# Performance work log

Measured on AMD Instinct MI355X. Metric: run time of the kernel, lower is better.

The kernel has to match this reference:

```python
import jax, jax.numpy as jnp
import numpy as np
from functools import partial

THRESHOLD = 2.0  # CannyEdgeNet(threshold=2.0)

# ---- fixed (non-learned) Canny filters, as in CannyEdgePytorch ----

def _gaussian_1d(size=5, std=1.0):
    x = np.arange(size) - (size - 1) / 2.0
    g = np.exp(-0.5 * (x / std) ** 2)
    g = g / g.sum()
    return g.astype(np.float32)

_G = _gaussian_1d(5, 1.0)
GAUSS_H = jnp.asarray(_G.reshape(1, 1, 1, 5))   # (O,I,kh,kw)
GAUSS_V = jnp.asarray(_G.reshape(1, 1, 5, 1))
_SOBEL = np.array([[1, 0, -1], [2, 0, -2], [1, 0, -1]], dtype=np.float32)
SOBEL_H = jnp.asarray(_SOBEL.reshape(1, 1, 3, 3))      # d/dx
SOBEL_V = jnp.asarray(_SOBEL.T.reshape(1, 1, 3, 3))    # d/dy
# 8 orientation-NMS filters: center minus neighbor at 0,45,...,315 degrees
_DIRS = np.zeros((8, 1, 3, 3), dtype=np.float32)
_NBR = [(1, 2), (2, 2), (2, 1), (2, 0), (1, 0), (0, 0), (0, 1), (0, 2)]
for _k, (_r, _c) in enumerate(_NBR):
    _DIRS[_k, 0, 1, 1] = 1.0
    _DIRS[_k, 0, _r, _c] = -1.0
DIR_FILTERS = jnp.asarray(_DIRS)

_DN = ('NCHW', 'OIHW', 'NCHW')

def _conv(x, w, pad):
    return jax.lax.conv_general_dilated(x, w, (1, 1), pad, dimension_numbers=_DN)


def canny_thresholded(img):
    """img: [N,3,H,W] -> thresholded thin edges [N,1,H,W]."""
    N, C, H, W = img.shape
    x = img.reshape(N * C, 1, H, W)
    # separable gaussian blur (per channel)
    blur = _conv(_conv(x, GAUSS_H, [(0, 0), (2, 2)]), GAUSS_V, [(2, 2), (0, 0)])
    gx = _conv(blur, SOBEL_H, [(1, 1), (1, 1)]).reshape(N, C, H, W)
    gy = _conv(blur, SOBEL_V, [(1, 1), (1, 1)]).reshape(N, C, H, W)
    # per-channel magnitudes summed over RGB, as in the original
    grad_mag = jnp.sqrt(gx * gx + gy * gy).sum(axis=1, keepdims=True)  # [N,1,H,W]
    gx_s = gx.sum(axis=1, keepdims=True)
    gy_s = gy.sum(axis=1, keepdims=True)
    ori = jnp.arctan2(gy_s, gx_s) * (180.0 / np.pi) + 180.0
    ori = jnp.round(ori / 45.0) * 45.0
    # orientation-dependent non-maximum suppression
    all_filtered = _conv(grad_mag, DIR_FILTERS, [(1, 1), (1, 1)])  # [N,8,H,W]
    idx_pos = jnp.mod(ori / 45.0, 8.0).astype(jnp.int32)            # [N,1,H,W]
    idx_neg = jnp.mod(ori / 45.0 + 4.0, 8.0).astype(jnp.int32)
    pos = jnp.take_along_axis(all_filtered, idx_pos, axis=1)
    neg = jnp.take_along_axis(all_filtered, idx_neg, axis=1)
    is_max = jnp.minimum(pos, neg) > 0.0
    thin = jnp.where(is_max, grad_mag, 0.0)
    thresholded = jnp.where(thin < THRESHOLD, 0.0, thin)
    return thresholded


def setup_inputs() -> dict:
    key = jax.random.key(0)
    k1, k2 = jax.random.split(key)
    shape = (4, 16, 3, 256, 256)  # [B, T, C, H, W]
    data_input = jax.random.uniform(k1, shape, dtype=jnp.float32)
    model_output = jax.random.uniform(k2, shape, dtype=jnp.float32)
    return {"data_input": data_input, "model_output": model_output}


def reference(data_input, model_output):
    B, T, C, H, W = data_input.shape
    tgt = data_input.reshape(B * T, C, H, W)
    out = model_output.reshape(B * T, C, H, W)
    # edge extraction is under torch.no_grad() in the original
    e_out = jax.lax.stop_gradient(canny_thresholded(out))
    e_tgt = jax.lax.stop_gradient(canny_thresholded(tgt))
    # mean over per-frame L1 losses == global mean (all frames equal size)
    return jnp.mean(jnp.abs(e_out - e_tgt))
```

## Files before the change

kernel.cpp:

```cpp
#include <hip/hip_runtime.h>
#include <math.h>

#define HW   256
#define TR   16
#define TC   32
#define NBLK 8192
#define BR   24
#define HC   36
#define VR   20
#define GR   18
#define GC   34
#define GCP  35
#define NHALO 100
#define NG1  (BR * 9)
#define NG2  (VR * 9)

typedef float f32x2 __attribute__((ext_vector_type(2)));

namespace {
constexpr double kE2  = 0.13533528323661269189;
constexpr double kE05 = 0.60653065971263342360;
constexpr double kSum = 1.0 + 2.0 * kE2 + 2.0 * kE05;
constexpr float G0f = (float)(kE2 / kSum);
constexpr float G1f = (float)(kE05 / kSum);
constexpr float G2f = (float)(1.0 / kSum);
constexpr float T1  = 0.41421356237309503f;
constexpr float T2  = 2.41421356237309503f;
__device__ __forceinline__ float fast_sqrtf(float x) {
    return __builtin_amdgcn_sqrtf(x);
}
__device__ __forceinline__ int iclamp(int v, int lo, int hi) {
    return v < lo ? lo : (v > hi ? hi : v);
}
__device__ __forceinline__ f32x2 mk2(float x, float y) {
    f32x2 r; r.x = x; r.y = y; return r;
}
}

template<bool EDGE>
__device__ __forceinline__ float tile_body(
    const float* __restrict__ bA, const float* __restrict__ bB,
    const int tid, const int ty0, const int tx0,
    float* __restrict__ s_tmp, float* __restrict__ s_blur,
    float* __restrict__ s_grad)
{
    const int ox  = tid & 31;
    const int oy0 = (tid >> 5) * 2;

    const f32x2 g0p = mk2(G0f, G0f), g1p = mk2(G1f, G1f), g2p = mk2(G2f, G2f);

    const int  q9  = tid / 9;
    const int  c4  = (tid - 9 * q9) * 4;
    const int  stw = q9 * HC + c4;
    const bool a1on = (tid < NG1);
    const int  y1   = ty0 - 4 + q9;
    const bool y1ok = !EDGE || ((unsigned)y1 < HW);
    const int  x0   = tx0 - 4 + c4;
    const int  ga   = y1 * HW + (EDGE ? iclamp(x0, 0, HW - 4) : x0);
    const int  gb   = y1 * HW + (EDGE ? iclamp(x0 + 4, 0, HW - 4) : x0 + 4);
    const bool a2on = (tid < NG2);
    const int  y2   = ty0 - 2 + q9;
    const bool y2ok = !EDGE || ((unsigned)y2 < HW);
    const int  xb2  = tx0 - 2 + c4;
    const bool ok0 = !EDGE || ((unsigned)(xb2 + 0) < HW);
    const bool ok1 = !EDGE || ((unsigned)(xb2 + 1) < HW);
    const bool ok2 = !EDGE || ((unsigned)(xb2 + 2) < HW);
    const bool ok3 = !EDGE || ((unsigned)(xb2 + 3) < HW);
    const int  b3  = (oy0 + 1) * HC + (ox + 1);
    const int  gw  = (oy0 + 1) * GCP + (ox + 1);
    int h_r = 0, h_cc = 0;
    if (tid < 34)        { h_r = 0;            h_cc = tid; }
    else if (tid < 68)   { h_r = GR - 1;       h_cc = tid - 34; }
    else if (tid < 84)   { h_r = tid - 68 + 1; h_cc = 0; }
    else if (tid < NHALO){ h_r = tid - 84 + 1; h_cc = GC - 1; }
    const bool has_halo = (tid < NHALO);
    const bool h_in = !EDGE || (((unsigned)(ty0 - 1 + h_r) < HW) &&
                                ((unsigned)(tx0 - 1 + h_cc) < HW));
    const int  h_b  = h_r * HC + h_cc;
    const int  h_gw = h_r * GCP + h_cc;

    f32x2 e_first = mk2(0.f, 0.f);
    float acc = 0.0f;

    for (int img = 0; img < 2; ++img) {
        const float* base = (img == 0) ? bA : bB;
        f32x2 gxs2 = mk2(0.f, 0.f), gys2 = mk2(0.f, 0.f), gms2 = mk2(0.f, 0.f);
        float hmag = 0.0f;

        for (int c = 0; c < 3; ++c) {
            const float* plane = base + c * (HW * HW);

            if (a1on) {
                float4 o = make_float4(0.f, 0.f, 0.f, 0.f);
                if (y1ok) {
                    const float4 a = *(const float4*)(plane + ga);
                    const float4 b = *(const float4*)(plane + gb);
                    const f32x2 p0 = mk2(a.x, a.y), p1 = mk2(a.y, a.z);
                    const f32x2 p2 = mk2(a.z, a.w), p3 = mk2(a.w, b.x);
                    const f32x2 p4 = mk2(b.x, b.y);
                    const f32x2 q3 = mk2(b.y, b.z), q4 = mk2(b.z, b.w);
                    const f32x2 oxy = g0p*p0 + g1p*p1 + g2p*p2 + g1p*p3 + g0p*p4;
                    const f32x2 ozw = g0p*p2 + g1p*p3 + g2p*p4 + g1p*q3 + g0p*q4;
                    o.x = oxy.x; o.y = oxy.y; o.z = ozw.x; o.w = ozw.y;
                    if (EDGE) {
                        if (x0 < 0) {
                            o.x = G0f*a.x;
                            o.y = G1f*a.x + G0f*a.y;
                            o.z = G2f*a.x + G1f*a.y + G0f*a.z;
                            o.w = G1f*a.x + G2f*a.y + G1f*a.z + G0f*a.w;
                        } else if (x0 > HW - 8) {
                            o.x = G0f*a.x + G1f*a.y + G2f*a.z + G1f*a.w;
                            o.y = G0f*a.y + G1f*a.z + G2f*a.w;
                            o.z = G0f*a.z + G1f*a.w;
                            o.w = G0f*a.w;
                        }
                    }
                }
                *(float4*)&s_tmp[stw] = o;
            }
            __syncthreads();

            if (a2on) {
                float4 v = make_float4(0.f, 0.f, 0.f, 0.f);
                if (y2ok) {
                    const float4 t0 = *(const float4*)&s_tmp[stw];
                    const float4 t1 = *(const float4*)&s_tmp[stw + 1 * HC];
                    const float4 t2 = *(const float4*)&s_tmp[stw + 2 * HC];
                    const float4 t3 = *(const float4*)&s_tmp[stw + 3 * HC];
                    const float4 t4 = *(const float4*)&s_tmp[stw + 4 * HC];
                    const f32x2 vxy = g0p*mk2(t0.x,t0.y) + g1p*mk2(t1.x,t1.y)
                                    + g2p*mk2(t2.x,t2.y) + g1p*mk2(t3.x,t3.y)
                                    + g0p*mk2(t4.x,t4.y);
                    const f32x2 vzw = g0p*mk2(t0.z,t0.w) + g1p*mk2(t1.z,t1.w)
                                    + g2p*mk2(t2.z,t2.w) + g1p*mk2(t3.z,t3.w)
                                    + g0p*mk2(t4.z,t4.w);
                    v.x = ok0 ? vxy.x : 0.f;
                    v.y = ok1 ? vxy.y : 0.f;
                    v.z = ok2 ? vzw.x : 0.f;
                    v.w = ok3 ? vzw.y : 0.f;
                }
                *(float4*)&s_blur[stw] = v;
            }
            __syncthreads();

            {
                float cd[4], rs[4];
                #pragma unroll
                for (int r = 0; r < 4; ++r) {
                    const float* b = &s_blur[b3 + r * HC];
                    const float bl = b[0], bc = b[1], br = b[2];
                    cd[r] = bl - br;
                    rs[r] = bl + 2.0f * bc + br;
                }
                const f32x2 gx2 = mk2(cd[0], cd[1]) + 2.0f * mk2(cd[1], cd[2])
                                + mk2(cd[2], cd[3]);
                const f32x2 gy2 = mk2(rs[0], rs[1]) - mk2(rs[2], rs[3]);
                gxs2 += gx2;
                gys2 += gy2;
                const f32x2 m2 = gx2 * gx2 + gy2 * gy2;
                gms2 += mk2(fast_sqrtf(m2.x), fast_sqrtf(m2.y));
                s_grad[gw]       = gms2.x;
                s_grad[gw + GCP] = gms2.y;
            }

            if (has_halo) {
                float gmag = 0.0f;
                if (h_in) {
                    const float* b = &s_blur[h_b];
                    const float b00 = b[0],        b01 = b[1],          b02 = b[2];
                    const float b10 = b[HC],                            b12 = b[HC + 2];
                    const float b20 = b[2 * HC],   b21 = b[2 * HC + 1], b22 = b[2 * HC + 2];
                    const float gx = (b00 + 2.0f * b10 + b20) - (b02 + 2.0f * b12 + b22);
                    const float gy = (b00 + 2.0f * b01 + b02) - (b20 + 2.0f * b21 + b22);
                    gmag = fast_sqrtf(gx * gx + gy * gy);
                }
                hmag += gmag;
                s_grad[h_gw] = hmag;
            }
        }
        __syncthreads();

        f32x2 e2;
        #pragma unroll
        for (int k = 0; k < 2; ++k) {
            const float gc = (k == 0) ? gms2.x : gms2.y;
            const float gx = (k == 0) ? gxs2.x : gxs2.y;
            const float gy = (k == 0) ? gys2.x : gys2.y;
            const float ax = fabsf(gx), ay = fabsf(gy);
            int dy, dx;
            if (ay <= T1 * ax)      { dy = 0; dx = 1; }
            else if (ay >= T2 * ax) { dy = 1; dx = 0; }
            else                    { dy = 1; dx = ((gx > 0.0f) == (gy > 0.0f)) ? 1 : -1; }
            const int ci = gw + k * GCP;
            const float pos = gc - s_grad[ci + dy * GCP + dx];
            const float neg = gc - s_grad[ci - dy * GCP - dx];
            const float thin = (fminf(pos, neg) > 0.0f) ? gc : 0.0f;
            const float e    = (thin < 2.0f) ? 0.0f : thin;
            if (k == 0) e2.x = e; else e2.y = e;
        }
        if (img == 0) e_first = e2;
        else          acc += fabsf(e2.x - e_first.x) + fabsf(e2.y - e_first.y);
        __syncthreads();
    }
    return acc;
}

__global__ __launch_bounds__(256, 8)
void canny_tile_kernel(const float* __restrict__ imgA,
                       const float* __restrict__ imgB,
                       float* __restrict__ partials)
{
    __shared__ __align__(16) float s_tmp[BR * HC];
    __shared__ __align__(16) float s_blur[VR * HC];
    __shared__ float s_grad[GR * GCP];
    __shared__ float s_red[4];

    const int tid = threadIdx.x;
    const int bid = blockIdx.x;
    const int lg  = (bid & 7) * (NBLK / 8) + (bid >> 3);
    const int n    = lg >> 7;
    const int tile = lg & 127;
    const int rt   = tile >> 3;
    const int ct   = tile & 7;
    const int ty0  = rt * TR;
    const int tx0  = ct * TC;

    const float* bA = imgA + (size_t)n * 3 * (HW * HW);
    const float* bB = imgB + (size_t)n * 3 * (HW * HW);

    const bool interior = (rt >= 1) && (rt <= 14) && (ct >= 1) && (ct <= 6);

    float acc;
    if (interior) acc = tile_body<false>(bA, bB, tid, ty0, tx0, s_tmp, s_blur, s_grad);
    else          acc = tile_body<true >(bA, bB, tid, ty0, tx0, s_tmp, s_blur, s_grad);

    #pragma unroll
    for (int off = 32; off > 0; off >>= 1) acc += __shfl_down(acc, off, 64);
    if ((tid & 63) == 0) s_red[tid >> 6] = acc;
    __syncthreads();
    if (tid == 0) partials[bid] = (s_red[0] + s_red[1]) + (s_red[2] + s_red[3]);
}

__global__ void final_reduce_kernel(const float* __restrict__ partials,
                                    float* __restrict__ out)
{
    __shared__ float s_red[16];
    const int tid = threadIdx.x;
    const float4 a = *(const float4*)&partials[4 * tid];
    const float4 b = *(const float4*)&partials[4 * tid + 4096];
    float v = ((a.x + a.y) + (a.z + a.w)) + ((b.x + b.y) + (b.z + b.w));
    #pragma unroll
    for (int off = 32; off > 0; off >>= 1) v += __shfl_down(v, off, 64);
    if ((tid & 63) == 0) s_red[tid >> 6] = v;
    __syncthreads();
    if (tid == 0) {
        float s = 0.0f;
        #pragma unroll
        for (int j = 0; j < 16; ++j) s += s_red[j];
        out[0] = s * (1.0f / 4194304.0f);
    }
}

extern "C" void kernel_launch(void* const* d_in, const int* in_sizes, int n_in,
                              void* d_out, int out_size, void* d_ws, size_t ws_size,
                              hipStream_t stream)
{
    const float* tgt     = (const float*)d_in[0];
    const float* out_img = (const float*)d_in[1];
    float* partials = (float*)d_ws;

    canny_tile_kernel<<<NBLK, 256, 0, stream>>>(out_img, tgt, partials);
    final_reduce_kernel<<<1, 1024, 0, stream>>>(partials, (float*)d_out);
}
```

Measured before the change: 47.06 us.

## Double tile height to 32 rows with four outputs per thread

Tile height grows from 16 to 32 rows, halving the block count. Each thread now makes two passes through the horizontal and vertical blur stages and computes four output rows instead of two. This cuts the relative halo overhead: fewer redundant global loads and blur work for overlapping rows. It also drops the trailing barrier at the end of each image iteration. In exchange there is more register pressure, a larger shared-memory footprint, and fewer blocks to spread across CUs.

```diff
diff --git a/kernel.cpp b/kernel.cpp
--- a/kernel.cpp
+++ b/kernel.cpp
@@ -2,16 +2,16 @@
 #include <math.h>
 
 #define HW   256
-#define TR   16
+#define TR   32
 #define TC   32
-#define NBLK 8192
-#define BR   24
+#define NBLK 4096
+#define BR   40
 #define HC   36
-#define VR   20
-#define GR   18
+#define VR   36
+#define GR   34
 #define GC   34
 #define GCP  35
-#define NHALO 100
+#define NHALO 132
 #define NG1  (BR * 9)
 #define NG2  (VR * 9)
 
@@ -45,122 +45,142 @@
     float* __restrict__ s_grad)
 {
     const int ox  = tid & 31;
-    const int oy0 = (tid >> 5) * 2;
+    const int oy0 = (tid >> 5) * 4;
 
     const f32x2 g0p = mk2(G0f, G0f), g1p = mk2(G1f, G1f), g2p = mk2(G2f, G2f);
 
-    const int  q9  = tid / 9;
-    const int  c4  = (tid - 9 * q9) * 4;
-    const int  stw = q9 * HC + c4;
-    const bool a1on = (tid < NG1);
-    const int  y1   = ty0 - 4 + q9;
-    const bool y1ok = !EDGE || ((unsigned)y1 < HW);
-    const int  x0   = tx0 - 4 + c4;
-    const int  ga   = y1 * HW + (EDGE ? iclamp(x0, 0, HW - 4) : x0);
-    const int  gb   = y1 * HW + (EDGE ? iclamp(x0 + 4, 0, HW - 4) : x0 + 4);
-    const bool a2on = (tid < NG2);
-    const int  y2   = ty0 - 2 + q9;
-    const bool y2ok = !EDGE || ((unsigned)y2 < HW);
-    const int  xb2  = tx0 - 2 + c4;
-    const bool ok0 = !EDGE || ((unsigned)(xb2 + 0) < HW);
-    const bool ok1 = !EDGE || ((unsigned)(xb2 + 1) < HW);
-    const bool ok2 = !EDGE || ((unsigned)(xb2 + 2) < HW);
-    const bool ok3 = !EDGE || ((unsigned)(xb2 + 3) < HW);
+    int  stw[2], ga[2], gb[2], x0v[2];
+    bool y1ok[2], y2ok[2], okc[2][4];
+    #pragma unroll
+    for (int j = 0; j < 2; ++j) {
+        const int gg = tid + j * 256;
+        const int r  = gg / 9;
+        const int c4 = (gg - 9 * r) * 4;
+        stw[j] = r * HC + c4;
+        const int y1 = ty0 - 4 + r;
+        y1ok[j] = !EDGE || ((unsigned)y1 < HW);
+        const int x0 = tx0 - 4 + c4;
+        x0v[j] = x0;
+        ga[j] = y1 * HW + (EDGE ? iclamp(x0, 0, HW - 4) : x0);
+        gb[j] = y1 * HW + (EDGE ? iclamp(x0 + 4, 0, HW - 4) : x0 + 4);
+        const int y2 = ty0 - 2 + r;
+        y2ok[j] = !EDGE || ((unsigned)y2 < HW);
+        const int xb2 = tx0 - 2 + c4;
+        #pragma unroll
+        for (int t = 0; t < 4; ++t)
+            okc[j][t] = !EDGE || ((unsigned)(xb2 + t) < HW);
+    }
     const int  b3  = (oy0 + 1) * HC + (ox + 1);
     const int  gw  = (oy0 + 1) * GCP + (ox + 1);
     int h_r = 0, h_cc = 0;
-    if (tid < 34)        { h_r = 0;            h_cc = tid; }
-    else if (tid < 68)   { h_r = GR - 1;       h_cc = tid - 34; }
-    else if (tid < 84)   { h_r = tid - 68 + 1; h_cc = 0; }
-    else if (tid < NHALO){ h_r = tid - 84 + 1; h_cc = GC - 1; }
+    if (tid < 34)        { h_r = 0;             h_cc = tid; }
+    else if (tid < 68)   { h_r = GR - 1;        h_cc = tid - 34; }
+    else if (tid < 100)  { h_r = tid - 68 + 1;  h_cc = 0; }
+    else if (tid < NHALO){ h_r = tid - 100 + 1; h_cc = GC - 1; }
     const bool has_halo = (tid < NHALO);
     const bool h_in = !EDGE || (((unsigned)(ty0 - 1 + h_r) < HW) &&
                                 ((unsigned)(tx0 - 1 + h_cc) < HW));
     const int  h_b  = h_r * HC + h_cc;
     const int  h_gw = h_r * GCP + h_cc;
 
-    f32x2 e_first = mk2(0.f, 0.f);
+    float e_first[4];
     float acc = 0.0f;
 
     for (int img = 0; img < 2; ++img) {
         const float* base = (img == 0) ? bA : bB;
-        f32x2 gxs2 = mk2(0.f, 0.f), gys2 = mk2(0.f, 0.f), gms2 = mk2(0.f, 0.f);
+        f32x2 gxs01 = mk2(0.f,0.f), gxs23 = mk2(0.f,0.f);
+        f32x2 gys01 = mk2(0.f,0.f), gys23 = mk2(0.f,0.f);
+        f32x2 gms01 = mk2(0.f,0.f), gms23 = mk2(0.f,0.f);
         float hmag = 0.0f;
 
         for (int c = 0; c < 3; ++c) {
             const float* plane = base + c * (HW * HW);
 
-            if (a1on) {
-                float4 o = make_float4(0.f, 0.f, 0.f, 0.f);
-                if (y1ok) {
-                    const float4 a = *(const float4*)(plane + ga);
-                    const float4 b = *(const float4*)(plane + gb);
-                    const f32x2 p0 = mk2(a.x, a.y), p1 = mk2(a.y, a.z);
-                    const f32x2 p2 = mk2(a.z, a.w), p3 = mk2(a.w, b.x);
-                    const f32x2 p4 = mk2(b.x, b.y);
-                    const f32x2 q3 = mk2(b.y, b.z), q4 = mk2(b.z, b.w);
-                    const f32x2 oxy = g0p*p0 + g1p*p1 + g2p*p2 + g1p*p3 + g0p*p4;
-                    const f32x2 ozw = g0p*p2 + g1p*p3 + g2p*p4 + g1p*q3 + g0p*q4;
-                    o.x = oxy.x; o.y = oxy.y; o.z = ozw.x; o.w = ozw.y;
-                    if (EDGE) {
-                        if (x0 < 0) {
-                            o.x = G0f*a.x;
-                            o.y = G1f*a.x + G0f*a.y;
-                            o.z = G2f*a.x + G1f*a.y + G0f*a.z;
-                            o.w = G1f*a.x + G2f*a.y + G1f*a.z + G0f*a.w;
-                        } else if (x0 > HW - 8) {
-                            o.x = G0f*a.x + G1f*a.y + G2f*a.z + G1f*a.w;
-                            o.y = G0f*a.y + G1f*a.z + G2f*a.w;
-                            o.z = G0f*a.z + G1f*a.w;
-                            o.w = G0f*a.w;
+            #pragma unroll
+            for (int j = 0; j < 2; ++j) {
+                if (j == 0 || tid < NG1 - 256) {
+                    float4 o = make_float4(0.f, 0.f, 0.f, 0.f);
+                    if (y1ok[j]) {
+                        const float4 a = *(const float4*)(plane + ga[j]);
+                        const float4 b = *(const float4*)(plane + gb[j]);
+                        const f32x2 p0 = mk2(a.x, a.y), p1 = mk2(a.y, a.z);
+                        const f32x2 p2 = mk2(a.z, a.w), p3 = mk2(a.w, b.x);
+                        const f32x2 p4 = mk2(b.x, b.y);
+                        const f32x2 q3 = mk2(b.y, b.z), q4 = mk2(b.z, b.w);
+                        const f32x2 oxy = g0p*p0 + g1p*p1 + g2p*p2 + g1p*p3 + g0p*p4;
+                        const f32x2 ozw = g0p*p2 + g1p*p3 + g2p*p4 + g1p*q3 + g0p*q4;
+                        o.x = oxy.x; o.y = oxy.y; o.z = ozw.x; o.w = ozw.y;
+                        if (EDGE) {
+                            if (x0v[j] < 0) {
+                                o.x = G0f*a.x;
+                                o.y = G1f*a.x + G0f*a.y;
+                                o.z = G2f*a.x + G1f*a.y + G0f*a.z;
+                                o.w = G1f*a.x + G2f*a.y + G1f*a.z + G0f*a.w;
+                            } else if (x0v[j] > HW - 8) {
+                                o.x = G0f*a.x + G1f*a.y + G2f*a.z + G1f*a.w;
+                                o.y = G0f*a.y + G1f*a.z + G2f*a.w;
+                                o.z = G0f*a.z + G1f*a.w;
+                                o.w = G0f*a.w;
+                            }
                         }
                     }
-                }
-                *(float4*)&s_tmp[stw] = o;
+                    *(float4*)&s_tmp[stw[j]] = o;
+                }
             }
             __syncthreads();
 
-            if (a2on) {
-                float4 v = make_float4(0.f, 0.f, 0.f, 0.f);
-                if (y2ok) {
-                    const float4 t0 = *(const float4*)&s_tmp[stw];
-                    const float4 t1 = *(const float4*)&s_tmp[stw + 1 * HC];
-                    const float4 t2 = *(const float4*)&s_tmp[stw + 2 * HC];
-                    const float4 t3 = *(const float4*)&s_tmp[stw + 3 * HC];
-                    const float4 t4 = *(const float4*)&s_tmp[stw + 4 * HC];
-                    const f32x2 vxy = g0p*mk2(t0.x,t0.y) + g1p*mk2(t1.x,t1.y)
-                                    + g2p*mk2(t2.x,t2.y) + g1p*mk2(t3.x,t3.y)
-                                    + g0p*mk2(t4.x,t4.y);
-                    const f32x2 vzw = g0p*mk2(t0.z,t0.w) + g1p*mk2(t1.z,t1.w)
-                                    + g2p*mk2(t2.z,t2.w) + g1p*mk2(t3.z,t3.w)
-                                    + g0p*mk2(t4.z,t4.w);
-                    v.x = ok0 ? vxy.x : 0.f;
-                    v.y = ok1 ? vxy.y : 0.f;
-                    v.z = ok2 ? vzw.x : 0.f;
-                    v.w = ok3 ? vzw.y : 0.f;
-                }
-                *(float4*)&s_blur[stw] = v;
+            #pragma unroll
+            for (int j = 0; j < 2; ++j) {
+                if (j == 0 || tid < NG2 - 256) {
+                    float4 v = make_float4(0.f, 0.f, 0.f, 0.f);
+                    if (y2ok[j]) {
+                        const int w = stw[j];
+                        const float4 t0 = *(const float4*)&s_tmp[w];
+                        const float4 t1 = *(const float4*)&s_tmp[w + 1 * HC];
+                        const float4 t2 = *(const float4*)&s_tmp[w + 2 * HC];
+                        const float4 t3 = *(const float4*)&s_tmp[w + 3 * HC];
+                        const float4 t4 = *(const float4*)&s_tmp[w + 4 * HC];
+                        const f32x2 vxy = g0p*mk2(t0.x,t0.y) + g1p*mk2(t1.x,t1.y)
+                                        + g2p*mk2(t2.x,t2.y) + g1p*mk2(t3.x,t3.y)
+                                        + g0p*mk2(t4.x,t4.y);
+                        const f32x2 vzw = g0p*mk2(t0.z,t0.w) + g1p*mk2(t1.z,t1.w)
+                                        + g2p*mk2(t2.z,t2.w) + g1p*mk2(t3.z,t3.w)
+                                        + g0p*mk2(t4.z,t4.w);
+                        v.x = okc[j][0] ? vxy.x : 0.f;
+                        v.y = okc[j][1] ? vxy.y : 0.f;
+                        v.z = okc[j][2] ? vzw.x : 0.f;
+                        v.w = okc[j][3] ? vzw.y : 0.f;
+                    }
+                    *(float4*)&s_blur[stw[j]] = v;
+                }
             }
             __syncthreads();
 
             {
-                float cd[4], rs[4];
+                float cd[6], rs[6];
                 #pragma unroll
-                for (int r = 0; r < 4; ++r) {
+                for (int r = 0; r < 6; ++r) {
                     const float* b = &s_blur[b3 + r * HC];
                     const float bl = b[0], bc = b[1], br = b[2];
                     cd[r] = bl - br;
                     rs[r] = bl + 2.0f * bc + br;
                 }
-                const f32x2 gx2 = mk2(cd[0], cd[1]) + 2.0f * mk2(cd[1], cd[2])
-                                + mk2(cd[2], cd[3]);
-                const f32x2 gy2 = mk2(rs[0], rs[1]) - mk2(rs[2], rs[3]);
-                gxs2 += gx2;
-                gys2 += gy2;
-                const f32x2 m2 = gx2 * gx2 + gy2 * gy2;
-                gms2 += mk2(fast_sqrtf(m2.x), fast_sqrtf(m2.y));
-                s_grad[gw]       = gms2.x;
-                s_grad[gw + GCP] = gms2.y;
+                const f32x2 gx01 = mk2(cd[0], cd[1]) + 2.0f * mk2(cd[1], cd[2])
+                                 + mk2(cd[2], cd[3]);
+                const f32x2 gx23 = mk2(cd[2], cd[3]) + 2.0f * mk2(cd[3], cd[4])
+                                 + mk2(cd[4], cd[5]);
+                const f32x2 gy01 = mk2(rs[0], rs[1]) - mk2(rs[2], rs[3]);
+                const f32x2 gy23 = mk2(rs[2], rs[3]) - mk2(rs[4], rs[5]);
+                gxs01 += gx01; gxs23 += gx23;
+                gys01 += gy01; gys23 += gy23;
+                const f32x2 m01 = gx01 * gx01 + gy01 * gy01;
+                const f32x2 m23 = gx23 * gx23 + gy23 * gy23;
+                gms01 += mk2(fast_sqrtf(m01.x), fast_sqrtf(m01.y));
+                gms23 += mk2(fast_sqrtf(m23.x), fast_sqrtf(m23.y));
+                s_grad[gw]           = gms01.x;
+                s_grad[gw + GCP]     = gms01.y;
+                s_grad[gw + 2 * GCP] = gms23.x;
+                s_grad[gw + 3 * GCP] = gms23.y;
             }
 
             if (has_halo) {
@@ -180,12 +200,13 @@
         }
         __syncthreads();
 
-        f32x2 e2;
+        const float gcv[4] = {gms01.x, gms01.y, gms23.x, gms23.y};
+        const float gxv[4] = {gxs01.x, gxs01.y, gxs23.x, gxs23.y};
+        const float gyv[4] = {gys01.x, gys01.y, gys23.x, gys23.y};
         #pragma unroll
-        for (int k = 0; k < 2; ++k) {
-            const float gc = (k == 0) ? gms2.x : gms2.y;
-            const float gx = (k == 0) ? gxs2.x : gxs2.y;
-            const float gy = (k == 0) ? gys2.x : gys2.y;
+        for (int k = 0; k < 4; ++k) {
+            const float gc = gcv[k];
+            const float gx = gxv[k], gy = gyv[k];
             const float ax = fabsf(gx), ay = fabsf(gy);
             int dy, dx;
             if (ay <= T1 * ax)      { dy = 0; dx = 1; }
@@ -196,11 +217,9 @@
             const float neg = gc - s_grad[ci - dy * GCP - dx];
             const float thin = (fminf(pos, neg) > 0.0f) ? gc : 0.0f;
             const float e    = (thin < 2.0f) ? 0.0f : thin;
-            if (k == 0) e2.x = e; else e2.y = e;
+            if (img == 0) e_first[k] = e;
+            else          acc += fabsf(e - e_first[k]);
         }
-        if (img == 0) e_first = e2;
-        else          acc += fabsf(e2.x - e_first.x) + fabsf(e2.y - e_first.y);
-        __syncthreads();
     }
     return acc;
 }
@@ -218,8 +237,8 @@
     const int tid = threadIdx.x;
     const int bid = blockIdx.x;
     const int lg  = (bid & 7) * (NBLK / 8) + (bid >> 3);
-    const int n    = lg >> 7;
-    const int tile = lg & 127;
+    const int n    = lg >> 6;
+    const int tile = lg & 63;
     const int rt   = tile >> 3;
     const int ct   = tile & 7;
     const int ty0  = rt * TR;
@@ -228,7 +247,7 @@
     const float* bA = imgA + (size_t)n * 3 * (HW * HW);
     const float* bB = imgB + (size_t)n * 3 * (HW * HW);
 
-    const bool interior = (rt >= 1) && (rt <= 14) && (ct >= 1) && (ct <= 6);
+    const bool interior = (rt >= 1) && (rt <= 6) && (ct >= 1) && (ct <= 6);
 
     float acc;
     if (interior) acc = tile_body<false>(bA, bB, tid, ty0, tx0, s_tmp, s_blur, s_grad);
@@ -247,8 +266,7 @@
     __shared__ float s_red[16];
     const int tid = threadIdx.x;
     const float4 a = *(const float4*)&partials[4 * tid];
-    const float4 b = *(const float4*)&partials[4 * tid + 4096];
-    float v = ((a.x + a.y) + (a.z + a.w)) + ((b.x + b.y) + (b.z + b.w));
+    float v = (a.x + a.y) + (a.z + a.w);
     #pragma unroll
     for (int off = 32; off > 0; off >>= 1) v += __shfl_down(v, off, 64);
     if ((tid & 63) == 0) s_red[tid >> 6] = v;
```

Measured after the change: 50.95 us. +8.3%, slower.

## Process both images concurrently per channel with duplicated shared buffers

Applied to the files above, without the earlier changes.

Replaces the sequential two-image loop with a single channel loop that handles image A and image B side by side, using separate shared-memory buffers for each. This halves the number of block-wide barriers and issues twice as many independent global loads and ALU operations between barriers, which exposes more instruction-level parallelism. In exchange, LDS use per block roughly doubles and register pressure rises, which may lower occupancy under the 8-blocks-per-SM launch bound.

```diff
diff --git a/kernel.cpp b/kernel.cpp
--- a/kernel.cpp
+++ b/kernel.cpp
@@ -41,8 +41,9 @@
 __device__ __forceinline__ float tile_body(
     const float* __restrict__ bA, const float* __restrict__ bB,
     const int tid, const int ty0, const int tx0,
-    float* __restrict__ s_tmp, float* __restrict__ s_blur,
-    float* __restrict__ s_grad)
+    float* __restrict__ s_tmpA,  float* __restrict__ s_tmpB,
+    float* __restrict__ s_blurA, float* __restrict__ s_blurB,
+    float* __restrict__ s_gradA, float* __restrict__ s_gradB)
 {
     const int ox  = tid & 31;
     const int oy0 = (tid >> 5) * 2;
@@ -79,128 +80,209 @@
     const int  h_b  = h_r * HC + h_cc;
     const int  h_gw = h_r * GCP + h_cc;
 
-    f32x2 e_first = mk2(0.f, 0.f);
-    float acc = 0.0f;
-
-    for (int img = 0; img < 2; ++img) {
-        const float* base = (img == 0) ? bA : bB;
-        f32x2 gxs2 = mk2(0.f, 0.f), gys2 = mk2(0.f, 0.f), gms2 = mk2(0.f, 0.f);
-        float hmag = 0.0f;
-
-        for (int c = 0; c < 3; ++c) {
-            const float* plane = base + c * (HW * HW);
-
-            if (a1on) {
-                float4 o = make_float4(0.f, 0.f, 0.f, 0.f);
-                if (y1ok) {
-                    const float4 a = *(const float4*)(plane + ga);
-                    const float4 b = *(const float4*)(plane + gb);
-                    const f32x2 p0 = mk2(a.x, a.y), p1 = mk2(a.y, a.z);
-                    const f32x2 p2 = mk2(a.z, a.w), p3 = mk2(a.w, b.x);
-                    const f32x2 p4 = mk2(b.x, b.y);
-                    const f32x2 q3 = mk2(b.y, b.z), q4 = mk2(b.z, b.w);
+    f32x2 gxsA = mk2(0.f,0.f), gysA = mk2(0.f,0.f), gmsA = mk2(0.f,0.f);
+    f32x2 gxsB = mk2(0.f,0.f), gysB = mk2(0.f,0.f), gmsB = mk2(0.f,0.f);
+    float hmA = 0.f, hmB = 0.f;
+
+    for (int c = 0; c < 3; ++c) {
+        const float* pA = bA + c * (HW * HW);
+        const float* pB = bB + c * (HW * HW);
+
+        if (a1on) {
+            float4 oA = make_float4(0.f,0.f,0.f,0.f);
+            float4 oB = make_float4(0.f,0.f,0.f,0.f);
+            if (y1ok) {
+                const float4 aA = *(const float4*)(pA + ga);
+                const float4 bA4 = *(const float4*)(pA + gb);
+                const float4 aB = *(const float4*)(pB + ga);
+                const float4 bB4 = *(const float4*)(pB + gb);
+                {
+                    const f32x2 p0 = mk2(aA.x, aA.y), p1 = mk2(aA.y, aA.z);
+                    const f32x2 p2 = mk2(aA.z, aA.w), p3 = mk2(aA.w, bA4.x);
+                    const f32x2 p4 = mk2(bA4.x, bA4.y);
+                    const f32x2 q3 = mk2(bA4.y, bA4.z), q4 = mk2(bA4.z, bA4.w);
                     const f32x2 oxy = g0p*p0 + g1p*p1 + g2p*p2 + g1p*p3 + g0p*p4;
                     const f32x2 ozw = g0p*p2 + g1p*p3 + g2p*p4 + g1p*q3 + g0p*q4;
-                    o.x = oxy.x; o.y = oxy.y; o.z = ozw.x; o.w = ozw.y;
-                    if (EDGE) {
-                        if (x0 < 0) {
-                            o.x = G0f*a.x;
-                            o.y = G1f*a.x + G0f*a.y;
-                            o.z = G2f*a.x + G1f*a.y + G0f*a.z;
-                            o.w = G1f*a.x + G2f*a.y + G1f*a.z + G0f*a.w;
-                        } else if (x0 > HW - 8) {
-                            o.x = G0f*a.x + G1f*a.y + G2f*a.z + G1f*a.w;
-                            o.y = G0f*a.y + G1f*a.z + G2f*a.w;
-                            o.z = G0f*a.z + G1f*a.w;
-                            o.w = G0f*a.w;
-                        }
+                    oA.x = oxy.x; oA.y = oxy.y; oA.z = ozw.x; oA.w = ozw.y;
+                }
+                {
+                    const f32x2 p0 = mk2(aB.x, aB.y), p1 = mk2(aB.y, aB.z);
+                    const f32x2 p2 = mk2(aB.z, aB.w), p3 = mk2(aB.w, bB4.x);
+                    const f32x2 p4 = mk2(bB4.x, bB4.y);
+                    const f32x2 q3 = mk2(bB4.y, bB4.z), q4 = mk2(bB4.z, bB4.w);
+                    const f32x2 oxy = g0p*p0 + g1p*p1 + g2p*p2 + g1p*p3 + g0p*p4;
+                    const f32x2 ozw = g0p*p2 + g1p*p3 + g2p*p4 + g1p*q3 + g0p*q4;
+                    oB.x = oxy.x; oB.y = oxy.y; oB.z = ozw.x; oB.w = ozw.y;
+                }
+                if (EDGE) {
+                    if (x0 < 0) {
+                        oA.x = G0f*aA.x;
+                        oA.y = G1f*aA.x + G0f*aA.y;
+                        oA.z = G2f*aA.x + G1f*aA.y + G0f*aA.z;
+                        oA.w = G1f*aA.x + G2f*aA.y + G1f*aA.z + G0f*aA.w;
+                        oB.x = G0f*aB.x;
+                        oB.y = G1f*aB.x + G0f*aB.y;
+                        oB.z = G2f*aB.x + G1f*aB.y + G0f*aB.z;
+                        oB.w = G1f*aB.x + G2f*aB.y + G1f*aB.z + G0f*aB.w;
+                    } else if (x0 > HW - 8) {
+                        oA.x = G0f*aA.x + G1f*aA.y + G2f*aA.z + G1f*aA.w;
+                        oA.y = G0f*aA.y + G1f*aA.z + G2f*aA.w;
+                        oA.z = G0f*aA.z + G1f*aA.w;
+                        oA.w = G0f*aA.w;
+                        oB.x = G0f*aB.x + G1f*aB.y + G2f*aB.z + G1f*aB.w;
+                        oB.y = G0f*aB.y + G1f*aB.z + G2f*aB.w;
+                        oB.z = G0f*aB.z + G1f*aB.w;
+                        oB.w = G0f*aB.w;
                     }
                 }
-                *(float4*)&s_tmp[stw] = o;
-            }
-            __syncthreads();
-
-            if (a2on) {
-                float4 v = make_float4(0.f, 0.f, 0.f, 0.f);
-                if (y2ok) {
-                    const float4 t0 = *(const float4*)&s_tmp[stw];
-                    const float4 t1 = *(const float4*)&s_tmp[stw + 1 * HC];
-                    const float4 t2 = *(const float4*)&s_tmp[stw + 2 * HC];
-                    const float4 t3 = *(const float4*)&s_tmp[stw + 3 * HC];
-                    const float4 t4 = *(const float4*)&s_tmp[stw + 4 * HC];
+            }
+            *(float4*)&s_tmpA[stw] = oA;
+            *(float4*)&s_tmpB[stw] = oB;
+        }
+        __syncthreads();
+
+        if (a2on) {
+            float4 vA = make_float4(0.f,0.f,0.f,0.f);
+            float4 vB = make_float4(0.f,0.f,0.f,0.f);
+            if (y2ok) {
+                {
+                    const float4 t0 = *(const float4*)&s_tmpA[stw];
+                    const float4 t1 = *(const float4*)&s_tmpA[stw + 1 * HC];
+                    const float4 t2 = *(const float4*)&s_tmpA[stw + 2 * HC];
+                    const float4 t3 = *(const float4*)&s_tmpA[stw + 3 * HC];
+                    const float4 t4 = *(const float4*)&s_tmpA[stw + 4 * HC];
                     const f32x2 vxy = g0p*mk2(t0.x,t0.y) + g1p*mk2(t1.x,t1.y)
                                     + g2p*mk2(t2.x,t2.y) + g1p*mk2(t3.x,t3.y)
                                     + g0p*mk2(t4.x,t4.y);
                     const f32x2 vzw = g0p*mk2(t0.z,t0.w) + g1p*mk2(t1.z,t1.w)
                                     + g2p*mk2(t2.z,t2.w) + g1p*mk2(t3.z,t3.w)
                                     + g0p*mk2(t4.z,t4.w);
-                    v.x = ok0 ? vxy.x : 0.f;
-                    v.y = ok1 ? vxy.y : 0.f;
-                    v.z = ok2 ? vzw.x : 0.f;
-                    v.w = ok3 ? vzw.y : 0.f;
-                }
-                *(float4*)&s_blur[stw] = v;
-            }
-            __syncthreads();
-
+                    vA.x = ok0 ? vxy.x : 0.f;
+                    vA.y = ok1 ? vxy.y : 0.f;
+                    vA.z = ok2 ? vzw.x : 0.f;
+                    vA.w = ok3 ? vzw.y : 0.f;
+                }
+                {
+                    const float4 t0 = *(const float4*)&s_tmpB[stw];
+                    const float4 t1 = *(const float4*)&s_tmpB[stw + 1 * HC];
+                    const float4 t2 = *(const float4*)&s_tmpB[stw + 2 * HC];
+                    const float4 t3 = *(const float4*)&s_tmpB[stw + 3 * HC];
+                    const float4 t4 = *(const float4*)&s_tmpB[stw + 4 * HC];
+                    const f32x2 vxy = g0p*mk2(t0.x,t0.y) + g1p*mk2(t1.x,t1.y)
+                                    + g2p*mk2(t2.x,t2.y) + g1p*mk2(t3.x,t3.y)
+                                    + g0p*mk2(t4.x,t4.y);
+                    const f32x2 vzw = g0p*mk2(t0.z,t0.w) + g1p*mk2(t1.z,t1.w)
+                                    + g2p*mk2(t2.z,t2.w) + g1p*mk2(t3.z,t3.w)
+                                    + g0p*mk2(t4.z,t4.w);
+                    vB.x = ok0 ? vxy.x : 0.f;
+                    vB.y = ok1 ? vxy.y : 0.f;
+                    vB.z = ok2 ? vzw.x : 0.f;
+                    vB.w = ok3 ? vzw.y : 0.f;
+                }
+            }
+            *(float4*)&s_blurA[stw] = vA;
+            *(float4*)&s_blurB[stw] = vB;
+        }
+        __syncthreads();
+
+        {
+            float cdA0, cdA1, cdA2, cdA3, rsA0, rsA1, rsA2, rsA3;
+            float cdB0, cdB1, cdB2, cdB3, rsB0, rsB1, rsB2, rsB3;
             {
-                float cd[4], rs[4];
-                #pragma unroll
-                for (int r = 0; r < 4; ++r) {
-                    const float* b = &s_blur[b3 + r * HC];
-                    const float bl = b[0], bc = b[1], br = b[2];
-                    cd[r] = bl - br;
-                    rs[r] = bl + 2.0f * bc + br;
-                }
-                const f32x2 gx2 = mk2(cd[0], cd[1]) + 2.0f * mk2(cd[1], cd[2])
-                                + mk2(cd[2], cd[3]);
-                const f32x2 gy2 = mk2(rs[0], rs[1]) - mk2(rs[2], rs[3]);
-                gxs2 += gx2;
-                gys2 += gy2;
-                const f32x2 m2 = gx2 * gx2 + gy2 * gy2;
-                gms2 += mk2(fast_sqrtf(m2.x), fast_sqrtf(m2.y));
-                s_grad[gw]       = gms2.x;
-                s_grad[gw + GCP] = gms2.y;
-            }
-
-            if (has_halo) {
-                float gmag = 0.0f;
-                if (h_in) {
-                    const float* b = &s_blur[h_b];
-                    const float b00 = b[0],        b01 = b[1],          b02 = b[2];
-                    const float b10 = b[HC],                            b12 = b[HC + 2];
-                    const float b20 = b[2 * HC],   b21 = b[2 * HC + 1], b22 = b[2 * HC + 2];
-                    const float gx = (b00 + 2.0f * b10 + b20) - (b02 + 2.0f * b12 + b22);
-                    const float gy = (b00 + 2.0f * b01 + b02) - (b20 + 2.0f * b21 + b22);
-                    gmag = fast_sqrtf(gx * gx + gy * gy);
-                }
-                hmag += gmag;
-                s_grad[h_gw] = hmag;
-            }
-        }
-        __syncthreads();
-
-        f32x2 e2;
-        #pragma unroll
-        for (int k = 0; k < 2; ++k) {
-            const float gc = (k == 0) ? gms2.x : gms2.y;
-            const float gx = (k == 0) ? gxs2.x : gxs2.y;
-            const float gy = (k == 0) ? gys2.x : gys2.y;
+                const float* b = &s_blurA[b3];
+                float bl, bc, br;
+                bl=b[0]; bc=b[1]; br=b[2]; cdA0=bl-br; rsA0=bl+2.f*bc+br; b+=HC;
+                bl=b[0]; bc=b[1]; br=b[2]; cdA1=bl-br; rsA1=bl+2.f*bc+br; b+=HC;
+                bl=b[0]; bc=b[1]; br=b[2]; cdA2=bl-br; rsA2=bl+2.f*bc+br; b+=HC;
+                bl=b[0]; bc=b[1]; br=b[2]; cdA3=bl-br; rsA3=bl+2.f*bc+br;
+            }
+            {
+                const float* b = &s_blurB[b3];
+                float bl, bc, br;
+                bl=b[0]; bc=b[1]; br=b[2]; cdB0=bl-br; rsB0=bl+2.f*bc+br; b+=HC;
+                bl=b[0]; bc=b[1]; br=b[2]; cdB1=bl-br; rsB1=bl+2.f*bc+br; b+=HC;
+                bl=b[0]; bc=b[1]; br=b[2]; cdB2=bl-br; rsB2=bl+2.f*bc+br; b+=HC;
+                bl=b[0]; bc=b[1]; br=b[2]; cdB3=bl-br; rsB3=bl+2.f*bc+br;
+            }
+            const f32x2 gxA = mk2(cdA0, cdA1) + 2.0f * mk2(cdA1, cdA2) + mk2(cdA2, cdA3);
+            const f32x2 gyA = mk2(rsA0, rsA1) - mk2(rsA2, rsA3);
+            const f32x2 gxB = mk2(cdB0, cdB1) + 2.0f * mk2(cdB1, cdB2) + mk2(cdB2, cdB3);
+            const f32x2 gyB = mk2(rsB0, rsB1) - mk2(rsB2, rsB3);
+            gxsA += gxA; gysA += gyA;
+            gxsB += gxB; gysB += gyB;
+            const f32x2 mA = gxA * gxA + gyA * gyA;
+            const f32x2 mB = gxB * gxB + gyB * gyB;
+            gmsA += mk2(fast_sqrtf(mA.x), fast_sqrtf(mA.y));
+            gmsB += mk2(fast_sqrtf(mB.x), fast_sqrtf(mB.y));
+            s_gradA[gw]       = gmsA.x;
+            s_gradA[gw + GCP] = gmsA.y;
+            s_gradB[gw]       = gmsB.x;
+            s_gradB[gw + GCP] = gmsB.y;
+        }
+
+        if (has_halo) {
+            float gmA = 0.0f, gmB = 0.0f;
+            if (h_in) {
+                {
+                    const float* b = &s_blurA[h_b];
+                    const float b00 = b[0],      b01 = b[1],        b02 = b[2];
+                    const float b10 = b[HC],                        b12 = b[HC + 2];
+                    const float b20 = b[2*HC],   b21 = b[2*HC + 1], b22 = b[2*HC + 2];
+                    const float gx = (b00 + 2.0f*b10 + b20) - (b02 + 2.0f*b12 + b22);
+                    const float gy = (b00 + 2.0f*b01 + b02) - (b20 + 2.0f*b21 + b22);
+                    gmA = fast_sqrtf(gx * gx + gy * gy);
+                }
+                {
+                    const float* b = &s_blurB[h_b];
+                    const float b00 = b[0],      b01 = b[1],        b02 = b[2];
+                    const float b10 = b[HC],                        b12 = b[HC + 2];
+                    const float b20 = b[2*HC],   b21 = b[2*HC + 1], b22 = b[2*HC + 2];
+                    const float gx = (b00 + 2.0f*b10 + b20) - (b02 + 2.0f*b12 + b22);
+                    const float gy = (b00 + 2.0f*b01 + b02) - (b20 + 2.0f*b21 + b22);
+                    gmB = fast_sqrtf(gx * gx + gy * gy);
+                }
+            }
+            hmA += gmA; hmB += gmB;
+            s_gradA[h_gw] = hmA;
+            s_gradB[h_gw] = hmB;
+        }
+    }
+    __syncthreads();
+
+    float acc = 0.0f;
+    #pragma unroll
+    for (int k = 0; k < 2; ++k) {
+        const int ci = gw + k * GCP;
+        float eA, eB;
+        {
+            const float gc = (k == 0) ? gmsA.x : gmsA.y;
+            const float gx = (k == 0) ? gxsA.x : gxsA.y;
+            const float gy = (k == 0) ? gysA.x : gysA.y;
             const float ax = fabsf(gx), ay = fabsf(gy);
             int dy, dx;
             if (ay <= T1 * ax)      { dy = 0; dx = 1; }
             else if (ay >= T2 * ax) { dy = 1; dx = 0; }
             else                    { dy = 1; dx = ((gx > 0.0f) == (gy > 0.0f)) ? 1 : -1; }
-            const int ci = gw + k * GCP;
-            const float pos = gc - s_grad[ci + dy * GCP + dx];
-            const float neg = gc - s_grad[ci - dy * GCP - dx];
+            const float pos = gc - s_gradA[ci + dy * GCP + dx];
+            const float neg = gc - s_gradA[ci - dy * GCP - dx];
             const float thin = (fminf(pos, neg) > 0.0f) ? gc : 0.0f;
-            const float e    = (thin < 2.0f) ? 0.0f : thin;
-            if (k == 0) e2.x = e; else e2.y = e;
-        }
-        if (img == 0) e_first = e2;
-        else          acc += fabsf(e2.x - e_first.x) + fabsf(e2.y - e_first.y);
-        __syncthreads();
+            eA = (thin < 2.0f) ? 0.0f : thin;
+        }
+        {
+            const float gc = (k == 0) ? gmsB.x : gmsB.y;
+            const float gx = (k == 0) ? gxsB.x : gxsB.y;
+            const float gy = (k == 0) ? gysB.x : gysB.y;
+            const float ax = fabsf(gx), ay = fabsf(gy);
+            int dy, dx;
+            if (ay <= T1 * ax)      { dy = 0; dx = 1; }
+            else if (ay >= T2 * ax) { dy = 1; dx = 0; }
+            else                    { dy = 1; dx = ((gx > 0.0f) == (gy > 0.0f)) ? 1 : -1; }
+            const float pos = gc - s_gradB[ci + dy * GCP + dx];
+            const float neg = gc - s_gradB[ci - dy * GCP - dx];
+            const float thin = (fminf(pos, neg) > 0.0f) ? gc : 0.0f;
+            eB = (thin < 2.0f) ? 0.0f : thin;
+        }
+        acc += fabsf(eA - eB);
     }
     return acc;
 }
@@ -210,9 +292,12 @@
                        const float* __restrict__ imgB,
                        float* __restrict__ partials)
 {
-    __shared__ __align__(16) float s_tmp[BR * HC];
-    __shared__ __align__(16) float s_blur[VR * HC];
-    __shared__ float s_grad[GR * GCP];
+    __shared__ __align__(16) float s_tmpA[BR * HC];
+    __shared__ __align__(16) float s_tmpB[BR * HC];
+    __shared__ __align__(16) float s_blurA[VR * HC];
+    __shared__ __align__(16) float s_blurB[VR * HC];
+    __shared__ float s_gradA[GR * GCP];
+    __shared__ float s_gradB[GR * GCP];
     __shared__ float s_red[4];
 
     const int tid = threadIdx.x;
@@ -231,8 +316,12 @@
     const bool interior = (rt >= 1) && (rt <= 14) && (ct >= 1) && (ct <= 6);
 
     float acc;
-    if (interior) acc = tile_body<false>(bA, bB, tid, ty0, tx0, s_tmp, s_blur, s_grad);
-    else          acc = tile_body<true >(bA, bB, tid, ty0, tx0, s_tmp, s_blur, s_grad);
+    if (interior) acc = tile_body<false>(bA, bB, tid, ty0, tx0,
+                                         s_tmpA, s_tmpB, s_blurA, s_blurB,
+                                         s_gradA, s_gradB);
+    else          acc = tile_body<true >(bA, bB, tid, ty0, tx0,
+                                         s_tmpA, s_tmpB, s_blurA, s_blurB,
+                                         s_gradA, s_gradB);
 
     #pragma unroll
     for (int off = 32; off > 0; off >>= 1) acc += __shfl_down(acc, off, 64);
```

After: 49.13 us. 4.4% more time.
